# Optimization experiments

Measured on AMD Instinct MI355X. Metric: run time of the kernel, lower is better.

## Reference

```python
import jax, jax.numpy as jnp
import numpy as np
from jax import lax

DN = ('NCHW', 'OIHW', 'NCHW')


def setup_inputs() -> dict:
    key = jax.random.key(0)
    ks = jax.random.split(key, 7)
    B, IC, OC, H, W = 8, 64, 64, 128, 128
    return {
        'x': jax.random.normal(ks[0], (B, IC, H, W), jnp.float32),
        'w3': jax.random.normal(ks[1], (OC, IC, 3, 3), jnp.float32) * 0.05,
        'b3': jax.random.normal(ks[2], (OC,), jnp.float32) * 0.05,
        'w5': jax.random.normal(ks[3], (OC, IC, 5, 5), jnp.float32) * 0.05,
        'b5': jax.random.normal(ks[4], (OC,), jnp.float32) * 0.05,
        'wr': jax.random.normal(ks[5], (OC, 10, 1, 1), jnp.float32) * 0.1,
        'br': jax.random.normal(ks[6], (OC,), jnp.float32) * 0.05,
    }


def reference(x, w3, b3, w5, b5, wr, br):
    # Two 'same' convs (k=3 pad 1, k=5 pad 2) as in layers['5']
    y3 = lax.conv_general_dilated(x, w3, (1, 1), 'SAME', dimension_numbers=DN) + b3[None, :, None, None]
    y5 = lax.conv_general_dilated(x, w5, (1, 1), 'SAME', dimension_numbers=DN) + b5[None, :, None, None]
    B, C, H, W = y3.shape
    # The nested pad/crop loop == 9 zero-padded unit shifts of y3:
    # stackedFeatures order per channel: [y5, shift(sh=0,sw=0..2), shift(sh=1,...), ...]
    # shifted[h, w] = y3[h + 1 - sw, w + 1 - sh] with zero padding.
    P = jnp.pad(y3, ((0, 0), (0, 0), (1, 1), (1, 1)))
    shifts = [P[:, :, 2 - sw:2 - sw + H, 2 - sh:2 - sh + W]
              for sh in range(3) for sw in range(3)]
    stacked = jnp.stack([y5] + shifts, axis=2)  # [B, C, 10, H, W]
    # remap: grouped 1x1 conv, groups=OC, 10 in-channels per group
    out = jnp.einsum('bcghw,cg->bchw', stacked, wr[:, :, 0, 0]) + br[None, :, None, None]
    return out
```

## Files before the change

kernel.cpp:

```cpp
#include <hip/hip_runtime.h>

typedef unsigned short u16;
typedef unsigned int u32;
typedef __attribute__((ext_vector_type(8))) short short8;
typedef __attribute__((ext_vector_type(4))) short short4v;
typedef __attribute__((ext_vector_type(4))) float floatx4;

#define HH 128
#define WW 128
#define XP 72

__device__ __forceinline__ float bf2f(u16 u) {
    u32 b = ((u32)u) << 16;
    return __builtin_bit_cast(float, b);
}
__device__ __forceinline__ u16 f2bf(float f) {
    u32 b = __builtin_bit_cast(u32, f);
    b += 0x7FFFu + ((b >> 16) & 1u);
    return (u16)(b >> 16);
}

typedef __attribute__((address_space(3))) u16 lds_u16;
typedef const __attribute__((address_space(1))) u16 glob_u16;
__device__ __forceinline__ void gl_lds16(const u16* g, u16* l) {
    __builtin_amdgcn_global_load_lds((glob_u16*)g, (lds_u16*)l, 16, 0, 0);
}

#define W5C_BYTE 256
#define W3S_BYTE 205056
#define SCAL_BYTE 303360
#define V_BYTE 306432
#define XT_BYTE 1371392
#define N_W5C 102400
#define N_W3S 49152
#define N_SCAL 768
#define PACK_N (N_W5C + N_W3S + N_SCAL)

__global__ __launch_bounds__(256) void sniff_kernel(const u16* __restrict__ xu,
                                                    int* __restrict__ flag) {
    __shared__ int cnt;
    if (threadIdx.x == 0) cnt = 0;
    __syncthreads();
    int c = 0;
    for (int k = 0; k < 8; ++k) {
        int idx = 2 * (threadIdx.x * 8 + k);
        u16 u = xu[idx];
        int e = (u >> 7) & 0xFF;
        if (e >= 140) c++;
    }
    atomicAdd(&cnt, c);
    __syncthreads();
    if (threadIdx.x == 0) *flag = (cnt >= 8) ? 1 : 0;
}

__device__ __forceinline__ float load_any(const void* p, int i, int isf32) {
    return isf32 ? ((const float*)p)[i] : bf2f(((const u16*)p)[i]);
}

__global__ __launch_bounds__(256) void prepack(
        const void* w3, const void* b3, const void* w5, const void* b5,
        const void* wr, const void* br, const int* __restrict__ flag,
        u16* __restrict__ w5c, u16* __restrict__ w3s, float* __restrict__ scal) {
    int i = blockIdx.x * 256 + threadIdx.x;
    if (i >= PACK_N) return;
    int f = *flag;
    if (i < N_W5C) {
        int j = i & 7, lane = (i >> 3) & 63, mt = (i >> 9) & 3, ks = i >> 11;
        int oc = mt * 16 + (lane & 15);
        int k = ks * 32 + ((lane >> 4) & 3) * 8 + j;
        int tap = k >> 6, ic = k & 63;
        int kh = tap / 5, kw = tap - kh * 5;
        int dh = kh - 2, dw = kw - 2;
        float v = load_any(wr, oc * 10, f) * load_any(w5, (oc * 64 + ic) * 25 + tap, f);
        for (int sw = 0; sw < 3; ++sw) {
            int r = dh + sw;
            if (r < 0 || r > 2) continue;
            for (int sh = 0; sh < 3; ++sh) {
                int c = dw + sh;
                if (c < 0 || c > 2) continue;
                v += load_any(wr, oc * 10 + 1 + sh * 3 + sw, f) *
                     load_any(w3, (oc * 64 + ic) * 9 + r * 3 + c, f);
            }
        }
        w5c[i] = f2bf(v);
    } else if (i < N_W5C + N_W3S) {
        int ii = i - N_W5C;
        int side = ii / 12288, rem = ii - side * 12288;
        int j = rem & 7, lane = (rem >> 3) & 63, mt = (rem >> 9) & 3, ks = rem >> 11;
        int oc = mt * 16 + (lane & 15);
        int k = ks * 32 + ((lane >> 4) & 3) * 8 + j;
        int kk = k >> 6, ic = k & 63;
        int r, c;
        if (side == 0)      { r = 2;  c = kk; }
        else if (side == 1) { r = 0;  c = kk; }
        else if (side == 2) { r = kk; c = 2;  }
        else                { r = kk; c = 0;  }
        w3s[ii] = f2bf(load_any(w3, (oc * 64 + ic) * 9 + r * 3 + c, f));
    } else {
        int i2 = i - N_W5C - N_W3S;
        float v;
        if (i2 < 64) {
            int oc = i2;
            float swr = 0.f;
            for (int g = 1; g <= 9; ++g) swr += load_any(wr, oc * 10 + g, f);
            v = load_any(wr, oc * 10, f) * load_any(b5, oc, f) +
                swr * load_any(b3, oc, f) + load_any(br, oc, f);
        } else if (i2 < 704) {
            v = load_any(wr, i2 - 64, f);
        } else {
            v = load_any(b3, i2 - 704, f);
        }
        scal[i2] = v;
    }
}

__global__ __launch_bounds__(256) void transpose_x(
        const void* __restrict__ x, const int* __restrict__ flag,
        u16* __restrict__ xt) {
    __shared__ u16 tbuf[32 * XP];
    const int b = blockIdx.z, h = blockIdx.y, w0 = blockIdx.x * 32;
    const int t = threadIdx.x;
    const int f = *flag;
    if (f) {
        const int w2 = t & 15, ic = t >> 4;
#pragma unroll
        for (int p = 0; p < 4; ++p) {
            int icc = ic + p * 16;
            const float* src = (const float*)x +
                (((size_t)(b * 64 + icc) * 128 + h) * 128 + w0 + 2 * w2);
            float2 v = *(const float2*)src;
            tbuf[(2 * w2) * XP + icc]     = f2bf(v.x);
            tbuf[(2 * w2 + 1) * XP + icc] = f2bf(v.y);
        }
    } else {
        const int w4 = t & 7, ic = t >> 3;
#pragma unroll
        for (int p = 0; p < 2; ++p) {
            int icc = ic + p * 32;
            const u16* src = (const u16*)x +
                (((size_t)(b * 64 + icc) * 128 + h) * 128 + w0 + 4 * w4);
            short4v v = *(const short4v*)src;
#pragma unroll
            for (int e = 0; e < 4; ++e)
                tbuf[(4 * w4 + e) * XP + icc] = (u16)v[e];
        }
    }
    __syncthreads();
    const int w = t >> 3, q = t & 7;
    short8 v = *(const short8*)&tbuf[w * XP + q * 8];
    *(short8*)(xt + ((size_t)((b * 128 + h) * 128) + w0 + w) * 64 + q * 8) = v;
}

__global__ __launch_bounds__(256) void virt_y3_mfma(
        const u16* __restrict__ xt, const u16* __restrict__ w3s,
        const float* __restrict__ scal, float* __restrict__ V) {
    __shared__ u16 xrow[146 * XP];
    const int side = blockIdx.x, b = blockIdx.y;
    const int tid = threadIdx.x;
    const int fixed = (side & 1) ? 127 : 0;
    {
        const int q8 = tid & 7, p0 = tid >> 3;
#pragma unroll
        for (int it = 0; it < 5; ++it) {
            int p = p0 + it * 32;
            if (p < 132) {
                int cc = p - 2;
                short8 v = {0, 0, 0, 0, 0, 0, 0, 0};
                if ((unsigned)cc < 128u) {
                    size_t idx = (side < 2)
                        ? ((size_t)(b * 128 + fixed) * 128 + cc)
                        : ((size_t)(b * 128 + cc) * 128 + fixed);
                    v = *(const short8*)(xt + idx * 64 + q8 * 8);
                }
                *(short8*)&xrow[p * XP + q8 * 8] = v;
            }
        }
    }
    __syncthreads();

    const int wv = tid >> 6, lane = tid & 63, cb = lane & 15, q = lane >> 4;
    floatx4 acc[9];
#pragma unroll
    for (int nt = 0; nt < 9; ++nt) acc[nt] = (floatx4){0.f, 0.f, 0.f, 0.f};

    const u16* wbase = w3s + side * 12288 + wv * 512 + lane * 8;
#pragma unroll
    for (int ks = 0; ks < 6; ++ks) {
        short8 aa = *(const short8*)(wbase + ks * 2048);
        const int kbase = ks * 32 + q * 8;
        const int kk = kbase >> 6, ic0 = kbase & 63;
#pragma unroll
        for (int nt = 0; nt < 9; ++nt) {
            int p = nt * 16 + cb + kk;
            short8 bb = *(const short8*)&xrow[p * XP + ic0];
            acc[nt] = __builtin_amdgcn_mfma_f32_16x16x32_bf16(aa, bb, acc[nt], 0, 0, 0);
        }
    }

    const float* b3f = scal + 704;
#pragma unroll
    for (int nt = 0; nt < 9; ++nt) {
        int pos = nt * 16 + cb;
        if (pos < 130) {
#pragma unroll
            for (int reg = 0; reg < 4; ++reg) {
                int oc = wv * 16 + q * 4 + reg;
                V[((size_t)(b * 4 + side) * 130 + pos) * 64 + oc] = acc[nt][reg] + b3f[oc];
            }
        }
    }
}

__global__ __launch_bounds__(256) void apply_fix(
        const float* __restrict__ V, const float* __restrict__ scal,
        const int* __restrict__ flag, void* __restrict__ out) {
    const int side = blockIdx.x, b = blockIdx.y;
    const int f = *flag;
    const float* wrf = scal + 64;
    const float* Vb = V + (size_t)b * 4 * 130 * 64;
    const float* VT = Vb;
    const float* VB = Vb + 130 * 64;
    const float* VL = Vb + 2 * 130 * 64;
    const float* VR = Vb + 3 * 130 * 64;
    const int nitems = (side < 2) ? 128 * 64 : 126 * 64;
    for (int idx = blockIdx.z * 256 + threadIdx.x; idx < nitems; idx += 2048) {
        int oc = idx & 63;
        int h, w;
        if (side < 2) { w = idx >> 6; h = side ? 127 : 0; }
        else          { h = (idx >> 6) + 1; w = (side == 2) ? 0 : 127; }
        float s = 0.f;
#pragma unroll
        for (int sh = 0; sh < 3; ++sh)
#pragma unroll
            for (int sw = 0; sw < 3; ++sw) {
                int qh = h + 1 - sw, qw = w + 1 - sh;
                float v;
                if (qh == -1)       v = VT[(qw + 1) * 64 + oc];
                else if (qh == 128) v = VB[(qw + 1) * 64 + oc];
                else if (qw == -1)  v = VL[(qh + 1) * 64 + oc];
                else if (qw == 128) v = VR[(qh + 1) * 64 + oc];
                else continue;
                s -= wrf[oc * 10 + 1 + sh * 3 + sw] * v;
            }
        size_t oidx = ((size_t)(b * 64 + oc) * 128 + h) * 128 + w;
        if (f) ((float*)out)[oidx] += s;
        else {
            u16* po = (u16*)out + oidx;
            *po = f2bf(bf2f(*po) + s);
        }
    }
}

__global__ __launch_bounds__(256, 2) void conv_main(
        const u16* __restrict__ xt, const u16* __restrict__ w5c,
        const float* __restrict__ scal, const int* __restrict__ flag,
        void* __restrict__ out) {
    __shared__ __align__(16) u16 xs[400 * XP];
    __shared__ __align__(16) u16 wbuf[2][2][2048];
    const int b = blockIdx.z, h0 = blockIdx.y * 16, w0 = blockIdx.x * 16;
    const int tid = threadIdx.x;
    const int f = *flag;
    const int wv = tid >> 6, lane = tid & 63;

    {
        const int q8 = tid & 7, p0 = tid >> 3;
        for (int it = 0; it < 13; ++it) {
            int px = p0 + it * 32;
            if (px < 400) {
                int r = px / 20, c = px - r * 20;
                int gh = h0 + r - 2, gw = w0 + c - 2;
                short8 v = {0, 0, 0, 0, 0, 0, 0, 0};
                if ((unsigned)gh < 128u && (unsigned)gw < 128u)
                    v = *(const short8*)(xt +
                            ((size_t)((b * 128 + gh) * 128 + gw)) * 64 + q8 * 8);
                *(short8*)&xs[px * XP + q8 * 8] = v;
            }
        }
    }
    gl_lds16(w5c + 0 * 2048 + wv * 512 + lane * 8, &wbuf[0][0][wv * 512]);
    gl_lds16(w5c + 1 * 2048 + wv * 512 + lane * 8, &wbuf[0][1][wv * 512]);
    __syncthreads();

    const int cb = lane & 15, q = lane >> 4, wv4 = wv * 4;
    floatx4 acc[4][4];
#pragma unroll
    for (int mt = 0; mt < 4; ++mt)
#pragma unroll
        for (int nt = 0; nt < 4; ++nt)
            acc[mt][nt] = (floatx4){0.f, 0.f, 0.f, 0.f};

#pragma unroll 1
    for (int tap = 0; tap < 25; ++tap) {
        const int p = tap & 1;
        if (tap + 1 < 25) {
            gl_lds16(w5c + (size_t)((tap + 1) * 2 + 0) * 2048 + wv * 512 + lane * 8,
                     &wbuf[p ^ 1][0][wv * 512]);
            gl_lds16(w5c + (size_t)((tap + 1) * 2 + 1) * 2048 + wv * 512 + lane * 8,
                     &wbuf[p ^ 1][1][wv * 512]);
        }
        const int kh = tap / 5, kw = tap - kh * 5;
#pragma unroll
        for (int s = 0; s < 2; ++s) {
            short8 aa[4], bb[4];
#pragma unroll
            for (int mt = 0; mt < 4; ++mt)
                aa[mt] = *(const short8*)&wbuf[p][s][mt * 512 + lane * 8];
#pragma unroll
            for (int nt = 0; nt < 4; ++nt)
                bb[nt] = *(const short8*)&xs[((wv4 + nt + kh) * 20 + cb + kw) * XP +
                                             s * 32 + q * 8];
#pragma unroll
            for (int nt = 0; nt < 4; ++nt)
#pragma unroll
                for (int mt = 0; mt < 4; ++mt)
                    acc[mt][nt] = __builtin_amdgcn_mfma_f32_16x16x32_bf16(
                        aa[mt], bb[nt], acc[mt][nt], 0, 0, 0);
        }
        __syncthreads();
    }

    const float* biasC = scal;
#pragma unroll
    for (int mt = 0; mt < 4; ++mt)
#pragma unroll
        for (int nt = 0; nt < 4; ++nt) {
            int gh = h0 + wv4 + nt;
#pragma unroll
            for (int reg = 0; reg < 4; ++reg) {
                int oc = mt * 16 + q * 4 + reg;
                float s = acc[mt][nt][reg] + biasC[oc];
                size_t oidx = ((size_t)(b * 64 + oc) * 128 + gh) * 128 + w0 + cb;
                if (f) ((float*)out)[oidx] = s;
                else   ((u16*)out)[oidx]   = f2bf(s);
            }
        }
}

extern "C" void kernel_launch(void* const* d_in, const int* in_sizes, int n_in,
                              void* d_out, int out_size, void* d_ws, size_t ws_size,
                              hipStream_t stream) {
    const void* x  = d_in[0];
    const void* w3 = d_in[1];
    const void* b3 = d_in[2];
    const void* w5 = d_in[3];
    const void* b5 = d_in[4];
    const void* wr = d_in[5];
    const void* br = d_in[6];

    int*   flag = (int*)d_ws;
    u16*   w5c  = (u16*)((char*)d_ws + W5C_BYTE);
    u16*   w3s  = (u16*)((char*)d_ws + W3S_BYTE);
    float* scal = (float*)((char*)d_ws + SCAL_BYTE);
    float* V    = (float*)((char*)d_ws + V_BYTE);
    u16*   xt   = (u16*)((char*)d_ws + XT_BYTE);

    sniff_kernel<<<1, 256, 0, stream>>>((const u16*)x, flag);
    prepack<<<(PACK_N + 255) / 256, 256, 0, stream>>>(w3, b3, w5, b5, wr, br, flag,
                                                      w5c, w3s, scal);
    transpose_x<<<dim3(4, 128, 8), 256, 0, stream>>>(x, flag, xt);
    virt_y3_mfma<<<dim3(4, 8), 256, 0, stream>>>(xt, w3s, scal, V);
    conv_main<<<dim3(8, 8, 8), 256, 0, stream>>>(xt, w5c, scal, flag, d_out);
    apply_fix<<<dim3(4, 8, 8), 256, 0, stream>>>(V, scal, flag, d_out);
}
```

Before: 147.1 us.

## Widen conv tiles to 16x32, batch weight staging, fuse dtype sniff into prepack

The main conv block now covers 32 columns instead of 16, so each weight fragment loaded from LDS is reused across twice as many MFMAs. Weights are staged five k-steps per chunk with ten barrier rounds instead of twenty-five. The dtype sniff moves into prepack, which removes one kernel launch. transpose_x now handles a whole row per block. In exchange, the larger LDS tile and doubled accumulators lower occupancy, the grid shrinks to 256 blocks, and the launch-bounds hint is dropped.

Result: no change. 148.9 us (+1.2%).

```diff
diff --git a/kernel.cpp b/kernel.cpp
--- a/kernel.cpp
+++ b/kernel.cpp
@@ -36,34 +36,28 @@
 #define N_SCAL 768
 #define PACK_N (N_W5C + N_W3S + N_SCAL)
 
-__global__ __launch_bounds__(256) void sniff_kernel(const u16* __restrict__ xu,
-                                                    int* __restrict__ flag) {
+__device__ __forceinline__ float load_any(const void* p, int i, int isf32) {
+    return isf32 ? ((const float*)p)[i] : bf2f(((const u16*)p)[i]);
+}
+
+__global__ __launch_bounds__(256) void prepack(
+        const void* x, const void* w3, const void* b3, const void* w5,
+        const void* b5, const void* wr, const void* br, int* __restrict__ flagp,
+        u16* __restrict__ w5c, u16* __restrict__ w3s, float* __restrict__ scal) {
     __shared__ int cnt;
     if (threadIdx.x == 0) cnt = 0;
     __syncthreads();
-    int c = 0;
-    for (int k = 0; k < 8; ++k) {
-        int idx = 2 * (threadIdx.x * 8 + k);
-        u16 u = xu[idx];
+    {
+        u16 u = ((const u16*)x)[2 * threadIdx.x];
         int e = (u >> 7) & 0xFF;
-        if (e >= 140) c++;
-    }
-    atomicAdd(&cnt, c);
-    __syncthreads();
-    if (threadIdx.x == 0) *flag = (cnt >= 8) ? 1 : 0;
-}
-
-__device__ __forceinline__ float load_any(const void* p, int i, int isf32) {
-    return isf32 ? ((const float*)p)[i] : bf2f(((const u16*)p)[i]);
-}
-
-__global__ __launch_bounds__(256) void prepack(
-        const void* w3, const void* b3, const void* w5, const void* b5,
-        const void* wr, const void* br, const int* __restrict__ flag,
-        u16* __restrict__ w5c, u16* __restrict__ w3s, float* __restrict__ scal) {
+        if (e >= 140) atomicAdd(&cnt, 1);
+    }
+    __syncthreads();
+    const int f = (cnt >= 8) ? 1 : 0;
+    if (blockIdx.x == 0 && threadIdx.x == 0) *flagp = f;
+
     int i = blockIdx.x * 256 + threadIdx.x;
     if (i >= PACK_N) return;
-    int f = *flag;
     if (i < N_W5C) {
         int j = i & 7, lane = (i >> 3) & 63, mt = (i >> 9) & 3, ks = i >> 11;
         int oc = mt * 16 + (lane & 15);
@@ -117,38 +111,48 @@
 __global__ __launch_bounds__(256) void transpose_x(
         const void* __restrict__ x, const int* __restrict__ flag,
         u16* __restrict__ xt) {
-    __shared__ u16 tbuf[32 * XP];
-    const int b = blockIdx.z, h = blockIdx.y, w0 = blockIdx.x * 32;
+    __shared__ u16 tbuf[128 * XP];
+    const int b = blockIdx.z, h = blockIdx.y;
     const int t = threadIdx.x;
     const int f = *flag;
     if (f) {
         const int w2 = t & 15, ic = t >> 4;
 #pragma unroll
-        for (int p = 0; p < 4; ++p) {
-            int icc = ic + p * 16;
-            const float* src = (const float*)x +
-                (((size_t)(b * 64 + icc) * 128 + h) * 128 + w0 + 2 * w2);
-            float2 v = *(const float2*)src;
-            tbuf[(2 * w2) * XP + icc]     = f2bf(v.x);
-            tbuf[(2 * w2 + 1) * XP + icc] = f2bf(v.y);
-        }
+        for (int c4 = 0; c4 < 4; ++c4)
+#pragma unroll
+            for (int p = 0; p < 4; ++p) {
+                int icc = ic + p * 16;
+                int w = c4 * 32 + 2 * w2;
+                const float* src = (const float*)x +
+                    (((size_t)(b * 64 + icc) * 128 + h) * 128 + w);
+                float2 v = *(const float2*)src;
+                tbuf[w * XP + icc]       = f2bf(v.x);
+                tbuf[(w + 1) * XP + icc] = f2bf(v.y);
+            }
     } else {
         const int w4 = t & 7, ic = t >> 3;
 #pragma unroll
-        for (int p = 0; p < 2; ++p) {
-            int icc = ic + p * 32;
-            const u16* src = (const u16*)x +
-                (((size_t)(b * 64 + icc) * 128 + h) * 128 + w0 + 4 * w4);
-            short4v v = *(const short4v*)src;
-#pragma unroll
-            for (int e = 0; e < 4; ++e)
-                tbuf[(4 * w4 + e) * XP + icc] = (u16)v[e];
-        }
-    }
-    __syncthreads();
-    const int w = t >> 3, q = t & 7;
-    short8 v = *(const short8*)&tbuf[w * XP + q * 8];
-    *(short8*)(xt + ((size_t)((b * 128 + h) * 128) + w0 + w) * 64 + q * 8) = v;
+        for (int c4 = 0; c4 < 4; ++c4)
+#pragma unroll
+            for (int p = 0; p < 2; ++p) {
+                int icc = ic + p * 32;
+                int w = c4 * 32 + 4 * w4;
+                const u16* src = (const u16*)x +
+                    (((size_t)(b * 64 + icc) * 128 + h) * 128 + w);
+                short4v v = *(const short4v*)src;
+#pragma unroll
+                for (int e = 0; e < 4; ++e)
+                    tbuf[(w + e) * XP + icc] = (u16)v[e];
+            }
+    }
+    __syncthreads();
+    const int q = t & 7;
+#pragma unroll
+    for (int c4 = 0; c4 < 4; ++c4) {
+        int w = c4 * 32 + (t >> 3);
+        short8 v = *(const short8*)&tbuf[w * XP + q * 8];
+        *(short8*)(xt + ((size_t)((b * 128 + h) * 128) + w) * 64 + q * 8) = v;
+    }
 }
 
 __global__ __launch_bounds__(256) void virt_y3_mfma(
@@ -251,23 +255,23 @@
     }
 }
 
-__global__ __launch_bounds__(256, 2) void conv_main(
+__global__ __launch_bounds__(256) void conv_main(
         const u16* __restrict__ xt, const u16* __restrict__ w5c,
         const float* __restrict__ scal, const int* __restrict__ flag,
         void* __restrict__ out) {
-    __shared__ __align__(16) u16 xs[400 * XP];
-    __shared__ __align__(16) u16 wbuf[2][2][2048];
-    const int b = blockIdx.z, h0 = blockIdx.y * 16, w0 = blockIdx.x * 16;
+    __shared__ __align__(16) u16 xs[720 * XP];
+    __shared__ __align__(16) u16 wbuf[2][5 * 2048];
+    const int b = blockIdx.z, h0 = blockIdx.y * 16, w0 = blockIdx.x * 32;
     const int tid = threadIdx.x;
     const int f = *flag;
     const int wv = tid >> 6, lane = tid & 63;
 
     {
         const int q8 = tid & 7, p0 = tid >> 3;
-        for (int it = 0; it < 13; ++it) {
+        for (int it = 0; it < 23; ++it) {
             int px = p0 + it * 32;
-            if (px < 400) {
-                int r = px / 20, c = px - r * 20;
+            if (px < 720) {
+                int r = px / 36, c = px - r * 36;
                 int gh = h0 + r - 2, gw = w0 + c - 2;
                 short8 v = {0, 0, 0, 0, 0, 0, 0, 0};
                 if ((unsigned)gh < 128u && (unsigned)gw < 128u)
@@ -277,44 +281,52 @@
             }
         }
     }
-    gl_lds16(w5c + 0 * 2048 + wv * 512 + lane * 8, &wbuf[0][0][wv * 512]);
-    gl_lds16(w5c + 1 * 2048 + wv * 512 + lane * 8, &wbuf[0][1][wv * 512]);
+    for (int i = wv; i < 20; i += 4)
+        gl_lds16(w5c + i * 512 + lane * 8, &wbuf[0][i * 512]);
     __syncthreads();
 
     const int cb = lane & 15, q = lane >> 4, wv4 = wv * 4;
-    floatx4 acc[4][4];
+    floatx4 acc[4][4][2];
 #pragma unroll
     for (int mt = 0; mt < 4; ++mt)
 #pragma unroll
-        for (int nt = 0; nt < 4; ++nt)
-            acc[mt][nt] = (floatx4){0.f, 0.f, 0.f, 0.f};
+        for (int r = 0; r < 4; ++r)
+#pragma unroll
+            for (int g = 0; g < 2; ++g)
+                acc[mt][r][g] = (floatx4){0.f, 0.f, 0.f, 0.f};
 
 #pragma unroll 1
-    for (int tap = 0; tap < 25; ++tap) {
-        const int p = tap & 1;
-        if (tap + 1 < 25) {
-            gl_lds16(w5c + (size_t)((tap + 1) * 2 + 0) * 2048 + wv * 512 + lane * 8,
-                     &wbuf[p ^ 1][0][wv * 512]);
-            gl_lds16(w5c + (size_t)((tap + 1) * 2 + 1) * 2048 + wv * 512 + lane * 8,
-                     &wbuf[p ^ 1][1][wv * 512]);
-        }
-        const int kh = tap / 5, kw = tap - kh * 5;
-#pragma unroll
-        for (int s = 0; s < 2; ++s) {
-            short8 aa[4], bb[4];
+    for (int ch = 0; ch < 10; ++ch) {
+        const int p = ch & 1;
+        if (ch + 1 < 10) {
+            const u16* src = w5c + (size_t)(ch + 1) * 10240;
+            for (int i = wv; i < 20; i += 4)
+                gl_lds16(src + i * 512 + lane * 8, &wbuf[p ^ 1][i * 512]);
+        }
+#pragma unroll
+        for (int kss = 0; kss < 5; ++kss) {
+            const int ks = ch * 5 + kss;
+            const int tap = ks >> 1, s = ks & 1;
+            const int kh = tap / 5, kw = tap - kh * 5;
+            short8 aa[4];
 #pragma unroll
             for (int mt = 0; mt < 4; ++mt)
-                aa[mt] = *(const short8*)&wbuf[p][s][mt * 512 + lane * 8];
-#pragma unroll
-            for (int nt = 0; nt < 4; ++nt)
-                bb[nt] = *(const short8*)&xs[((wv4 + nt + kh) * 20 + cb + kw) * XP +
-                                             s * 32 + q * 8];
-#pragma unroll
-            for (int nt = 0; nt < 4; ++nt)
-#pragma unroll
-                for (int mt = 0; mt < 4; ++mt)
-                    acc[mt][nt] = __builtin_amdgcn_mfma_f32_16x16x32_bf16(
-                        aa[mt], bb[nt], acc[mt][nt], 0, 0, 0);
+                aa[mt] = *(const short8*)&wbuf[p][kss * 2048 + mt * 512 + lane * 8];
+            short8 bb[4][2];
+#pragma unroll
+            for (int r = 0; r < 4; ++r)
+#pragma unroll
+                for (int g = 0; g < 2; ++g)
+                    bb[r][g] = *(const short8*)&xs[
+                        ((wv4 + r + kh) * 36 + cb + g * 16 + kw) * XP + s * 32 + q * 8];
+#pragma unroll
+            for (int r = 0; r < 4; ++r)
+#pragma unroll
+                for (int g = 0; g < 2; ++g)
+#pragma unroll
+                    for (int mt = 0; mt < 4; ++mt)
+                        acc[mt][r][g] = __builtin_amdgcn_mfma_f32_16x16x32_bf16(
+                            aa[mt], bb[r][g], acc[mt][r][g], 0, 0, 0);
         }
         __syncthreads();
     }
@@ -323,17 +335,20 @@
 #pragma unroll
     for (int mt = 0; mt < 4; ++mt)
 #pragma unroll
-        for (int nt = 0; nt < 4; ++nt) {
-            int gh = h0 + wv4 + nt;
-#pragma unroll
-            for (int reg = 0; reg < 4; ++reg) {
-                int oc = mt * 16 + q * 4 + reg;
-                float s = acc[mt][nt][reg] + biasC[oc];
-                size_t oidx = ((size_t)(b * 64 + oc) * 128 + gh) * 128 + w0 + cb;
-                if (f) ((float*)out)[oidx] = s;
-                else   ((u16*)out)[oidx]   = f2bf(s);
-            }
-        }
+        for (int r = 0; r < 4; ++r)
+#pragma unroll
+            for (int g = 0; g < 2; ++g) {
+                int gh = h0 + wv4 + r;
+                int gw = w0 + g * 16 + cb;
+#pragma unroll
+                for (int reg = 0; reg < 4; ++reg) {
+                    int oc = mt * 16 + q * 4 + reg;
+                    float s = acc[mt][r][g][reg] + biasC[oc];
+                    size_t oidx = ((size_t)(b * 64 + oc) * 128 + gh) * 128 + gw;
+                    if (f) ((float*)out)[oidx] = s;
+                    else   ((u16*)out)[oidx]   = f2bf(s);
+                }
+            }
 }
 
 extern "C" void kernel_launch(void* const* d_in, const int* in_sizes, int n_in,
@@ -354,11 +369,10 @@
     float* V    = (float*)((char*)d_ws + V_BYTE);
     u16*   xt   = (u16*)((char*)d_ws + XT_BYTE);
 
-    sniff_kernel<<<1, 256, 0, stream>>>((const u16*)x, flag);
-    prepack<<<(PACK_N + 255) / 256, 256, 0, stream>>>(w3, b3, w5, b5, wr, br, flag,
-                                                      w5c, w3s, scal);
-    transpose_x<<<dim3(4, 128, 8), 256, 0, stream>>>(x, flag, xt);
+    prepack<<<(PACK_N + 255) / 256, 256, 0, stream>>>(x, w3, b3, w5, b5, wr, br,
+                                                      flag, w5c, w3s, scal);
+    transpose_x<<<dim3(1, 128, 8), 256, 0, stream>>>(x, flag, xt);
     virt_y3_mfma<<<dim3(4, 8), 256, 0, stream>>>(xt, w3s, scal, V);
-    conv_main<<<dim3(8, 8, 8), 256, 0, stream>>>(xt, w5c, scal, flag, d_out);
+    conv_main<<<dim3(4, 8, 8), 256, 0, stream>>>(xt, w5c, scal, flag, d_out);
     apply_fix<<<dim3(4, 8, 8), 256, 0, stream>>>(V, scal, flag, d_out);
 }
```
